# Kernel optimization log

Measured on AMD Instinct MI355X. Metric: run time of the kernel, lower is better.

Reference implementation:

```python
import jax, jax.numpy as jnp
import numpy as np

D_MODEL = 768
N_HEAD = 12
D_FF = 2048
KEEP_RATIO = 0.6
EPS = 1e-6


def rmsnorm(x, g):
    var = jnp.mean(x * x, axis=-1, keepdims=True)
    return x * jax.lax.rsqrt(var + EPS) * g


def setup_inputs() -> dict:
    key = jax.random.key(0)
    ks = jax.random.split(key, 16)
    B, S, D, F = 2, 2048, D_MODEL, D_FF
    s = 0.02
    inp = {
        "hidden": jax.random.normal(ks[0], (B, S, D), jnp.float32),
        "attn_mask": jnp.tril(jnp.ones((S, S), dtype=bool)),
        "temperature": 1,
        "wq": jax.random.normal(ks[1], (D, D), jnp.float32) * s,
        "wk": jax.random.normal(ks[2], (D, D), jnp.float32) * s,
        "wv": jax.random.normal(ks[3], (D, D), jnp.float32) * s,
        "wo": jax.random.normal(ks[4], (D, D), jnp.float32) * s,
        "w1": jax.random.normal(ks[5], (D, F), jnp.float32) * s,
        "w3": jax.random.normal(ks[6], (D, F), jnp.float32) * s,
        "w2": jax.random.normal(ks[7], (F, D), jnp.float32) * s,
        "g1": jnp.ones((D,), jnp.float32),
        "g2": jnp.ones((D,), jnp.float32),
        "w_mod": jax.random.normal(ks[8], (D,), jnp.float32) * s,
        "b_mod": jnp.zeros((), jnp.float32),
        "w_tok": jax.random.normal(ks[9], (D,), jnp.float32) * s,
        "b_tok": jnp.zeros((), jnp.float32),
        "w_gate": jax.random.normal(ks[10], (D, D), jnp.float32) * s,
        "b_gate": jnp.zeros((D,), jnp.float32),
    }
    return inp


def reference(hidden, attn_mask, temperature, wq, wk, wv, wo, w1, w3, w2,
              g1, g2, w_mod, b_mod, w_tok, b_tok, w_gate, b_gate):
    B, S, D = hidden.shape
    H = N_HEAD
    Dh = D // H

    # depth router: sigmoid(linear / temperature)
    depth_logits = jnp.einsum("bsd,d->bs", hidden, w_mod) + b_mod
    depth_probs = jax.nn.sigmoid(depth_logits / temperature)
    active = (depth_probs > 0.5).astype(hidden.dtype)[..., None]  # [B,S,1]

    normed = rmsnorm(hidden, g1)

    # token router: sigmoid scores, hard top-k keep mask at base keep ratio
    token_scores = jax.nn.sigmoid(jnp.einsum("bsd,d->bs", normed, w_tok) + b_tok)
    k = max(1, int(S * KEEP_RATIO))
    kth = jax.lax.top_k(token_scores, k)[0][:, -1:]  # [B,1]
    token_mask = (token_scores >= kth).astype(hidden.dtype)  # [B,S]

    # multi-head attention over normed
    q = jnp.einsum("bsd,de->bse", normed, wq).reshape(B, S, H, Dh)
    kk = jnp.einsum("bsd,de->bse", normed, wk).reshape(B, S, H, Dh)
    v = jnp.einsum("bsd,de->bse", normed, wv).reshape(B, S, H, Dh)
    logits = jnp.einsum("bqhd,bkhd->bhqk", q, kk) / jnp.sqrt(jnp.float32(Dh))
    logits = jnp.where(attn_mask[None, None, :, :], logits, jnp.float32(-1e9))
    probs = jax.nn.softmax(logits, axis=-1)
    ctx = jnp.einsum("bhqk,bkhd->bqhd", probs, v).reshape(B, S, D)
    attn_out = jnp.einsum("bsd,de->bse", ctx, wo)

    attn_out = attn_out * token_mask[..., None]
    hidden = hidden + attn_out * active  # dropout = identity (eval)

    # ACM gate: x * sigmoid(Wx + b)
    n2 = rmsnorm(hidden, g2)
    gated = n2 * jax.nn.sigmoid(jnp.einsum("bsd,de->bse", n2, w_gate) + b_gate)

    # SwiGLU MLP
    mlp = jnp.einsum("bsf,fd->bsd",
                     jax.nn.silu(jnp.einsum("bsd,df->bsf", gated, w1))
                     * jnp.einsum("bsd,df->bsf", gated, w3), w2)
    hidden = hidden + mlp * active
    return hidden, depth_probs, token_mask
```

## Files before the change

kernel.cpp:

```cpp
#include <hip/hip_runtime.h>


typedef float f32x4 __attribute__((ext_vector_type(4)));
typedef __bf16 bf16x8 __attribute__((ext_vector_type(8)));
typedef __bf16 bf16x4 __attribute__((ext_vector_type(4)));
typedef unsigned int u32;

#define DEV static __device__ __forceinline__

constexpr int SEQ = 2048, DIM = 768, NH = 12;
constexpr int KKEEP = 1228;

DEV f32x4 mfma16(bf16x8 a, bf16x8 b, f32x4 c) {
  return __builtin_amdgcn_mfma_f32_16x16x32_bf16(a, b, c, 0, 0, 0);
}
DEV float sigm(float x) { return 1.0f / (1.0f + __expf(-x)); }
DEV bf16x8 ld8(const __bf16* p) { return *reinterpret_cast<const bf16x8*>(p); }
DEV void st8(__bf16* p, bf16x8 v) { *reinterpret_cast<bf16x8*>(p) = v; }
DEV int swzo(int row, int u) { return row * 64 + ((u ^ (row & 7)) << 3); }

template <int NZ>
struct PtrPack { const float* s[NZ]; };

template <int NZ>
__global__ void k_transpose_castz(PtrPack<NZ> pp, __bf16* __restrict__ dst0,
                                  int K, int N, size_t dstride) {
  const float* __restrict__ src = pp.s[blockIdx.z];
  __bf16* __restrict__ dst = dst0 + (size_t)blockIdx.z * dstride;
  __shared__ float tile[32][33];
  const int tx = threadIdx.x, ty = threadIdx.y;
  const int n0 = blockIdx.x * 32, k0 = blockIdx.y * 32;
  for (int i = 0; i < 4; ++i)
    tile[ty + 8 * i][tx] = src[(size_t)(k0 + ty + 8 * i) * N + n0 + tx];
  __syncthreads();
  for (int i = 0; i < 4; ++i)
    dst[(size_t)(n0 + ty + 8 * i) * K + k0 + tx] = (__bf16)tile[tx][ty + 8 * i];
}

__global__ __launch_bounds__(256) void k_router(
    const float* __restrict__ hid, const float* __restrict__ g1,
    const float* __restrict__ wmod, const float* __restrict__ bmod,
    const float* __restrict__ wtok, const float* __restrict__ btok,
    const int* __restrict__ temp, __bf16* __restrict__ normed,
    float* __restrict__ depth_out, float* __restrict__ actF,
    float* __restrict__ tokL) {
  const int t = blockIdx.x, tid = threadIdx.x;
  const float* x = hid + (size_t)t * DIM;
  float xs[3], gs[3], ss = 0.f, dm = 0.f, dt = 0.f;
  for (int j = 0; j < 3; ++j) {
    const int i = tid + 256 * j;
    const float xv = x[i], g = g1[i];
    xs[j] = xv; gs[j] = g;
    ss += xv * xv;
    dm += xv * wmod[i];
    dt += xv * g * wtok[i];
  }
  for (int m = 32; m >= 1; m >>= 1) {
    ss += __shfl_xor(ss, m);
    dm += __shfl_xor(dm, m);
    dt += __shfl_xor(dt, m);
  }
  __shared__ float red[4][3];
  if ((tid & 63) == 0) { red[tid >> 6][0] = ss; red[tid >> 6][1] = dm; red[tid >> 6][2] = dt; }
  __syncthreads();
  ss = red[0][0] + red[1][0] + red[2][0] + red[3][0];
  dm = red[0][1] + red[1][1] + red[2][1] + red[3][1];
  dt = red[0][2] + red[1][2] + red[2][2] + red[3][2];
  const float rms = rsqrtf(ss / 768.0f + 1e-6f);
  if (tid == 0) {
    const int iv = temp[0];
    const float T = (iv > -100000 && iv < 100000) ? (float)iv : __int_as_float(iv);
    const float z = (dm + bmod[0]) / T;
    depth_out[t] = sigm(z);
    actF[t] = z > 0.0f ? 1.0f : 0.0f;
    tokL[t] = rms * dt + btok[0];
  }
  for (int j = 0; j < 3; ++j) {
    const int i = tid + 256 * j;
    normed[(size_t)t * DIM + i] = (__bf16)(xs[j] * rms * gs[j]);
  }
}

__global__ __launch_bounds__(256) void k_count(
    const float* __restrict__ tokL, float* __restrict__ kth_out) {
  const int b = blockIdx.y, tid = threadIdx.x;
  __shared__ float vals[2048];
  const float* L = tokL + (size_t)b * 2048;
#pragma unroll
  for (int j = 0; j < 8; ++j) vals[tid + 256 * j] = L[tid + 256 * j];
  __syncthreads();
  const int cand = blockIdx.x * 128 + (tid >> 1);
  const int half = tid & 1;
  const float e = vals[cand];
  int gt = 0, ge = 0;
  const float4* v4 = reinterpret_cast<const float4*>(vals) + half * 256;
#pragma unroll 8
  for (int j = 0; j < 256; ++j) {
    const float4 q = v4[j];
    gt += (q.x > e) + (q.y > e) + (q.z > e) + (q.w > e);
    ge += (q.x >= e) + (q.y >= e) + (q.z >= e) + (q.w >= e);
  }
  gt += __shfl_xor(gt, 1);
  ge += __shfl_xor(ge, 1);
  if (half == 0 && gt < KKEEP && KKEEP <= ge) kth_out[b] = e;
}

__global__ __launch_bounds__(256) void k_mask(
    const float* __restrict__ tokL, const float* __restrict__ kth,
    const float* __restrict__ actF, float* __restrict__ mask_out,
    float* __restrict__ maskact) {
  const int i = blockIdx.x * 256 + threadIdx.x;
  const int b = i >> 11;
  const float m = (tokL[i] >= kth[b]) ? 1.f : 0.f;
  mask_out[i] = m;
  maskact[i] = m * actF[i];
}

__global__ __launch_bounds__(256) void k_rmsnorm2(
    const float* __restrict__ h2, const float* __restrict__ g2,
    __bf16* __restrict__ n2) {
  const int t = blockIdx.x, tid = threadIdx.x;
  const float* x = h2 + (size_t)t * DIM;
  float xs[3], ss = 0.f;
  for (int j = 0; j < 3; ++j) { const float v = x[tid + 256 * j]; xs[j] = v; ss += v * v; }
  for (int m = 32; m >= 1; m >>= 1) ss += __shfl_xor(ss, m);
  __shared__ float red[4];
  if ((tid & 63) == 0) red[tid >> 6] = ss;
  __syncthreads();
  ss = red[0] + red[1] + red[2] + red[3];
  const float rms = rsqrtf(ss / 768.0f + 1e-6f);
  for (int j = 0; j < 3; ++j) {
    const int i = tid + 256 * j;
    n2[(size_t)t * DIM + i] = (__bf16)(xs[j] * rms * g2[i]);
  }
}

template <int EPI, int MI>
__global__ __launch_bounds__(256) void k_gemm(
    const __bf16* __restrict__ A, const __bf16* __restrict__ BT,
    int N, int K, size_t bt_stride, size_t out_stride,
    __bf16* __restrict__ outB, float* __restrict__ outF,
    const float* __restrict__ epF, const __bf16* __restrict__ epB,
    const float* __restrict__ rowsc, const float* __restrict__ bias) {
  constexpr int BM = MI * 32;
  __shared__ __align__(16) __bf16 As[BM * 64];
  __shared__ __align__(16) __bf16 Bs[128 * 64];
  const int tid = threadIdx.x;
  const int lane = tid & 63, w = tid >> 6;
  const int wr = w >> 1, wc = w & 1;
  const int f = lane & 15, e = lane >> 4;
  const int m0 = blockIdx.y * BM, n0 = blockIdx.x * 128;
  const __bf16* Bz = BT + (size_t)blockIdx.z * bt_stride;

  const int rowA = (MI == 4) ? (tid >> 1) : (tid >> 2);
  const int uA0  = (MI == 4) ? ((tid & 1) * 4) : ((tid & 3) * 2);
  const int rowB = tid >> 1, uB0 = (tid & 1) * 4;
  const __bf16* ApR = A + (size_t)(m0 + rowA) * K;
  const __bf16* BpR = Bz + (size_t)(n0 + rowB) * K;

  bf16x8 ya[MI], yb[4];
  auto LOADY = [&](int k0) {
#pragma unroll
    for (int j = 0; j < MI; ++j) ya[j] = ld8(ApR + k0 + (uA0 + j) * 8);
#pragma unroll
    for (int j = 0; j < 4; ++j) yb[j] = ld8(BpR + k0 + (uB0 + j) * 8);
  };
  auto STORE = [&]() {
#pragma unroll
    for (int j = 0; j < MI; ++j) st8(&As[swzo(rowA, uA0 + j)], ya[j]);
#pragma unroll
    for (int j = 0; j < 4; ++j) st8(&Bs[swzo(rowB, uB0 + j)], yb[j]);
  };

  f32x4 acc[MI][4] = {};
  LOADY(0);
  for (int k0 = 0; k0 < K; k0 += 64) {
    __syncthreads();
    STORE();
    if (k0 + 64 < K) LOADY(k0 + 64);
    __syncthreads();
    bf16x8 afl[MI], afh[MI], bfl[4], bfh[4];
#pragma unroll
    for (int mi = 0; mi < MI; ++mi) {
      const int row = wr * (MI * 16) + mi * 16 + f;
      afl[mi] = ld8(&As[swzo(row, e)]);
      afh[mi] = ld8(&As[swzo(row, e + 4)]);
    }
#pragma unroll
    for (int ni = 0; ni < 4; ++ni) {
      const int row = wc * 64 + ni * 16 + f;
      bfl[ni] = ld8(&Bs[swzo(row, e)]);
      bfh[ni] = ld8(&Bs[swzo(row, e + 4)]);
    }
#pragma unroll
    for (int mi = 0; mi < MI; ++mi)
#pragma unroll
      for (int ni = 0; ni < 4; ++ni) {
        acc[mi][ni] = mfma16(afl[mi], bfl[ni], acc[mi][ni]);
        acc[mi][ni] = mfma16(afh[mi], bfh[ni], acc[mi][ni]);
      }
  }
  const size_t oz = (size_t)blockIdx.z * out_stride;
  if constexpr (EPI == 5) {
    __bf16* vt = (__bf16*)outF;
    const bool isv = (blockIdx.z == 2);
#pragma unroll
    for (int mi = 0; mi < MI; ++mi)
#pragma unroll
      for (int ni = 0; ni < 4; ++ni) {
        const int row0 = m0 + wr * (MI * 16) + mi * 16 + e * 4;
        const int col = n0 + wc * 64 + ni * 16 + f;
        if (!isv) {
#pragma unroll
          for (int r2 = 0; r2 < 4; ++r2)
            outB[oz + (size_t)(row0 + r2) * N + col] = (__bf16)acc[mi][ni][r2];
        } else {
          bf16x4 pk;
#pragma unroll
          for (int r2 = 0; r2 < 4; ++r2) pk[r2] = (__bf16)acc[mi][ni][r2];
          *reinterpret_cast<bf16x4*>(&vt[(size_t)col * 4096 + row0]) = pk;
        }
      }
  } else {
#pragma unroll
    for (int mi = 0; mi < MI; ++mi)
#pragma unroll
      for (int ni = 0; ni < 4; ++ni)
#pragma unroll
        for (int r2 = 0; r2 < 4; ++r2) {
          const int row = m0 + wr * (MI * 16) + mi * 16 + e * 4 + r2;
          const int col = n0 + wc * 64 + ni * 16 + f;
          const size_t idx = (size_t)row * N + col;
          const float c = acc[mi][ni][r2];
          if constexpr (EPI == 0) {
            outB[oz + idx] = (__bf16)c;
          } else if constexpr (EPI == 1) {
            outF[idx] = epF[idx] + c * rowsc[row];
          } else if constexpr (EPI == 2) {
            outB[idx] = (__bf16)((float)epB[idx] * sigm(c + bias[col]));
          }
        }
  }
}

__global__ __launch_bounds__(256) void k_gemm13(
    const __bf16* __restrict__ A, const __bf16* __restrict__ B1T,
    const __bf16* __restrict__ B3T, __bf16* __restrict__ outT) {
  __shared__ __align__(16) __bf16 As[64 * 64];
  __shared__ __align__(16) __bf16 B1s[128 * 64];
  __shared__ __align__(16) __bf16 B3s[128 * 64];
  const int tid = threadIdx.x;
  const int lane = tid & 63, w = tid >> 6;
  const int wr = w >> 1, wc = w & 1;
  const int f = lane & 15, e = lane >> 4;
  const int m0 = blockIdx.y * 64, n0 = blockIdx.x * 128;
  const int rowA = tid >> 2, uA0 = (tid & 3) * 2;
  const int rowB = tid >> 1, uB0 = (tid & 1) * 4;
  const __bf16* ApR = A + (size_t)(m0 + rowA) * 768;
  const __bf16* B1R = B1T + (size_t)(n0 + rowB) * 768;
  const __bf16* B3R = B3T + (size_t)(n0 + rowB) * 768;

  bf16x8 ya[2], yb1[4], yb3[4];
  auto LOADY = [&](int k0) {
#pragma unroll
    for (int j = 0; j < 2; ++j) ya[j] = ld8(ApR + k0 + (uA0 + j) * 8);
#pragma unroll
    for (int j = 0; j < 4; ++j) yb1[j] = ld8(B1R + k0 + (uB0 + j) * 8);
#pragma unroll
    for (int j = 0; j < 4; ++j) yb3[j] = ld8(B3R + k0 + (uB0 + j) * 8);
  };
  auto STORE = [&]() {
#pragma unroll
    for (int j = 0; j < 2; ++j) st8(&As[swzo(rowA, uA0 + j)], ya[j]);
#pragma unroll
    for (int j = 0; j < 4; ++j) st8(&B1s[swzo(rowB, uB0 + j)], yb1[j]);
#pragma unroll
    for (int j = 0; j < 4; ++j) st8(&B3s[swzo(rowB, uB0 + j)], yb3[j]);
  };

  f32x4 acc1[2][4] = {}, acc3[2][4] = {};
  LOADY(0);
  for (int k0 = 0; k0 < 768; k0 += 64) {
    __syncthreads();
    STORE();
    if (k0 + 64 < 768) LOADY(k0 + 64);
    __syncthreads();
    bf16x8 afl[2], afh[2], bl[4], bh[4];
#pragma unroll
    for (int mi = 0; mi < 2; ++mi) {
      const int row = wr * 32 + mi * 16 + f;
      afl[mi] = ld8(&As[swzo(row, e)]);
      afh[mi] = ld8(&As[swzo(row, e + 4)]);
    }
#pragma unroll
    for (int ni = 0; ni < 4; ++ni) {
      const int row = wc * 64 + ni * 16 + f;
      bl[ni] = ld8(&B1s[swzo(row, e)]);
      bh[ni] = ld8(&B1s[swzo(row, e + 4)]);
    }
#pragma unroll
    for (int mi = 0; mi < 2; ++mi)
#pragma unroll
      for (int ni = 0; ni < 4; ++ni) {
        acc1[mi][ni] = mfma16(afl[mi], bl[ni], acc1[mi][ni]);
        acc1[mi][ni] = mfma16(afh[mi], bh[ni], acc1[mi][ni]);
      }
#pragma unroll
    for (int ni = 0; ni < 4; ++ni) {
      const int row = wc * 64 + ni * 16 + f;
      bl[ni] = ld8(&B3s[swzo(row, e)]);
      bh[ni] = ld8(&B3s[swzo(row, e + 4)]);
    }
#pragma unroll
    for (int mi = 0; mi < 2; ++mi)
#pragma unroll
      for (int ni = 0; ni < 4; ++ni) {
        acc3[mi][ni] = mfma16(afl[mi], bl[ni], acc3[mi][ni]);
        acc3[mi][ni] = mfma16(afh[mi], bh[ni], acc3[mi][ni]);
      }
  }
#pragma unroll
  for (int mi = 0; mi < 2; ++mi)
#pragma unroll
    for (int ni = 0; ni < 4; ++ni)
#pragma unroll
      for (int r2 = 0; r2 < 4; ++r2) {
        const int row = m0 + wr * 32 + mi * 16 + e * 4 + r2;
        const int col = n0 + wc * 64 + ni * 16 + f;
        const float u = acc1[mi][ni][r2];
        outT[(size_t)row * 2048 + col] = (__bf16)(u * sigm(u) * acc3[mi][ni][r2]);
      }
}

__global__ __launch_bounds__(256) void k_attn(
    const __bf16* __restrict__ qb, const __bf16* __restrict__ kb,
    const __bf16* __restrict__ vT, __bf16* __restrict__ Opart,
    float* __restrict__ ml) {
  __shared__ __bf16 Ks[64 * 64];
  __shared__ __bf16 Vt[64 * 64];
  __shared__ __bf16 Pl[4][16][72];
  const int tid = threadIdx.x, lane = tid & 63, w = tid >> 6;
  const int f = lane & 15, e = lane >> 4;
  const int idx = 79 - (int)blockIdx.x;
  int g4, rel;
  if (idx < 8)       { g4 = 0; rel = idx; }
  else if (idx < 24) { g4 = 1; rel = idx - 8; }
  else if (idx < 48) { g4 = 2; rel = idx - 24; }
  else               { g4 = 3; rel = idx - 48; }
  const int qt = (g4 << 3) + rel / (g4 + 1);
  const int c  = rel % (g4 + 1);
  const int bh = blockIdx.y;
  const int b = bh / NH, h = bh % NH;
  const int slot = bh * 80 + idx;
  const int q0 = qt * 64;
  const int kt0 = c * 8;
  const int ntile = min(8, qt + 1 - kt0);
  const size_t base = (size_t)b * SEQ * DIM + (size_t)h * 64;
  const float SCALE2 = 0.125f * 1.4426950408889634f;

  const int qrow = q0 + w * 16 + f;
  const bf16x8 aq0 = ld8(qb + base + (size_t)qrow * DIM + e * 8);
  const bf16x8 aq1 = ld8(qb + base + (size_t)qrow * DIM + 32 + e * 8);
  float lsum[4] = {0.f, 0.f, 0.f, 0.f};
  f32x4 cacc[4];
  for (int g = 0; g < 4; ++g) cacc[g] = f32x4{0.f, 0.f, 0.f, 0.f};

  const int r1 = tid >> 2, u0 = tid & 3;
  const __bf16* kp = kb + base + (size_t)r1 * DIM;
  const __bf16* vp = vT + (size_t)(h * 64 + r1) * 4096 + b * 2048;

  bf16x8 rk0 = ld8(kp + (size_t)(kt0 * 64) * DIM + u0 * 8);
  bf16x8 rk1 = ld8(kp + (size_t)(kt0 * 64) * DIM + (u0 + 4) * 8);
  bf16x8 rv0 = ld8(vp + kt0 * 64 + u0 * 8);
  bf16x8 rv1 = ld8(vp + kt0 * 64 + (u0 + 4) * 8);

  for (int tt = 0; tt < ntile; ++tt) {
    const int kt = kt0 + tt;
    __syncthreads();
    st8(&Ks[swzo(r1, u0)], rk0);  st8(&Ks[swzo(r1, u0 + 4)], rk1);
    st8(&Vt[swzo(r1, u0)], rv0);  st8(&Vt[swzo(r1, u0 + 4)], rv1);
    if (tt + 1 < ntile) {
      const size_t ko = (size_t)((kt + 1) * 64) * DIM;
      rk0 = ld8(kp + ko + u0 * 8);  rk1 = ld8(kp + ko + (u0 + 4) * 8);
      const int vo = (kt + 1) * 64;
      rv0 = ld8(vp + vo + u0 * 8);  rv1 = ld8(vp + vo + (u0 + 4) * 8);
    }
    __syncthreads();

    f32x4 sacc[4];
#pragma unroll
    for (int g = 0; g < 4; ++g) {
      const int row = g * 16 + f;
      f32x4 z = f32x4{0.f, 0.f, 0.f, 0.f};
      z = mfma16(aq0, ld8(&Ks[swzo(row, e)]), z);
      z = mfma16(aq1, ld8(&Ks[swzo(row, e + 4)]), z);
      sacc[g] = z;
    }
    const bool need_mask = (kt == qt);
    const int qg = q0 + w * 16 + e * 4;
    float p[4][4];
#pragma unroll
    for (int g = 0; g < 4; ++g) {
      const int kg = kt * 64 + g * 16 + f;
#pragma unroll
      for (int r = 0; r < 4; ++r) {
        const float pv = (need_mask && (kg > qg + r))
                             ? 0.f
                             : exp2f(sacc[g][r] * SCALE2);
        p[g][r] = pv;
        lsum[r] += pv;
      }
    }
#pragma unroll
    for (int g = 0; g < 4; ++g)
#pragma unroll
      for (int r = 0; r < 4; ++r) Pl[w][e * 4 + r][g * 16 + f] = (__bf16)p[g][r];
    const bf16x8 ap0 = ld8(&Pl[w][f][e * 8]);
    const bf16x8 ap1 = ld8(&Pl[w][f][32 + e * 8]);
#pragma unroll
    for (int g = 0; g < 4; ++g) {
      const int row = g * 16 + f;
      cacc[g] = mfma16(ap0, ld8(&Vt[swzo(row, e)]), cacc[g]);
      cacc[g] = mfma16(ap1, ld8(&Vt[swzo(row, e + 4)]), cacc[g]);
    }
  }
  for (int m = 1; m < 16; m <<= 1)
#pragma unroll
    for (int r = 0; r < 4; ++r) lsum[r] += __shfl_xor(lsum[r], m);
  if (f == 0) {
#pragma unroll
    for (int r = 0; r < 4; ++r)
      ml[(size_t)slot * 64 + w * 16 + e * 4 + r] = lsum[r];
  }
#pragma unroll
  for (int g = 0; g < 4; ++g)
#pragma unroll
    for (int r = 0; r < 4; ++r) {
      const int row = w * 16 + e * 4 + r;
      Opart[(size_t)slot * 4096 + row * 64 + g * 16 + f] = (__bf16)cacc[g][r];
    }
}

__global__ __launch_bounds__(256) void k_attn_combine(
    const __bf16* __restrict__ Opart, const float* __restrict__ ml,
    __bf16* __restrict__ ctxb) {
  const int qt = blockIdx.x, bh = blockIdx.y;
  const int b = bh / NH, h = bh % NH;
  const int g = qt >> 3;
  const int sb = bh * 80 + 4 * g * (g + 1) + (qt & 7) * (g + 1);
  const int nch = g + 1;
  const int row = threadIdx.x >> 2, dh0 = (threadIdx.x & 3) * 16;

  float ltot = 0.f;
  float acc[16];
#pragma unroll
  for (int j = 0; j < 16; ++j) acc[j] = 0.f;
  for (int cc = 0; cc < nch; ++cc) {
    ltot += ml[(size_t)(sb + cc) * 64 + row];
    const __bf16* op = Opart + (size_t)(sb + cc) * 4096 + row * 64 + dh0;
    const bf16x8 o0 = ld8(op), o1 = ld8(op + 8);
#pragma unroll
    for (int j = 0; j < 8; ++j) {
      acc[j] += (float)o0[j];
      acc[8 + j] += (float)o1[j];
    }
  }
  const float rl = 1.0f / ltot;
  bf16x8 w0, w1;
#pragma unroll
  for (int j = 0; j < 8; ++j) {
    w0[j] = (__bf16)(acc[j] * rl);
    w1[j] = (__bf16)(acc[8 + j] * rl);
  }
  const size_t base = (size_t)b * SEQ * DIM + (size_t)h * 64;
  __bf16* dst = ctxb + base + (size_t)(qt * 64 + row) * DIM + dh0;
  st8(dst, w0);
  st8(dst + 8, w1);
}

extern "C" void kernel_launch(void* const* d_in, const int* in_sizes, int n_in,
                              void* d_out, int out_size, void* d_ws, size_t ws_size,
                              hipStream_t stream) {
  const float* hid   = (const float*)d_in[0];
  const int*   temp  = (const int*)d_in[2];
  const float* wq    = (const float*)d_in[3];
  const float* wk    = (const float*)d_in[4];
  const float* wv    = (const float*)d_in[5];
  const float* wo    = (const float*)d_in[6];
  const float* w1    = (const float*)d_in[7];
  const float* w3    = (const float*)d_in[8];
  const float* w2    = (const float*)d_in[9];
  const float* g1    = (const float*)d_in[10];
  const float* g2    = (const float*)d_in[11];
  const float* wmod  = (const float*)d_in[12];
  const float* bmod  = (const float*)d_in[13];
  const float* wtok  = (const float*)d_in[14];
  const float* btok  = (const float*)d_in[15];
  const float* wgate = (const float*)d_in[16];
  const float* bgate = (const float*)d_in[17];

  char* ws = (char*)d_ws;
  __bf16* WT = (__bf16*)ws;
  const size_t oWQ = 0, oWK = 589824, oWV = 1179648, oWO = 1769472,
               oWG = 2359296, oW1 = 2949120, oW3 = 4521984, oW2 = 6094848;
  __bf16* qbuf   = (__bf16*)(ws + 15335424);
  __bf16* kbuf   = qbuf + 3145728;
  __bf16* vTbuf  = kbuf + 3145728;
  __bf16* normed = (__bf16*)(ws + 34209792);
  __bf16* ctxb   = normed + 3145728;
  __bf16* n2buf  = ctxb + 3145728;
  __bf16* tbuf   = normed;
  float*  h2     = (float*)(ws + 53084160);
  __bf16* gated  = (__bf16*)(ws + 65667072);
  __bf16* Opart  = (__bf16*)(ws + 53084160);
  float*  mlbuf  = (float*)(ws + 68812800);
  float*  tokL   = (float*)(ws + 71958528);
  float*  actF   = tokL + 4096;
  float*  maskact = actF + 4096;
  float*  kthbuf  = maskact + 4096;

  float* dout = (float*)d_out;
  float* out_hidden = dout;
  float* out_depth  = dout + 3145728;
  float* out_mask   = dout + 3145728 + 4096;

  const dim3 tb(32, 8);
  PtrPack<5> p5; p5.s[0]=wq; p5.s[1]=wk; p5.s[2]=wv; p5.s[3]=wo; p5.s[4]=wgate;
  k_transpose_castz<5><<<dim3(24, 24, 5), tb, 0, stream>>>(p5, WT + oWQ, 768, 768, 589824);
  PtrPack<2> p2; p2.s[0]=w1; p2.s[1]=w3;
  k_transpose_castz<2><<<dim3(64, 24, 2), tb, 0, stream>>>(p2, WT + oW1, 768, 2048, 1572864);
  PtrPack<1> p1; p1.s[0]=w2;
  k_transpose_castz<1><<<dim3(24, 64, 1), tb, 0, stream>>>(p1, WT + oW2, 2048, 768, 0);

  k_router<<<4096, 256, 0, stream>>>(hid, g1, wmod, bmod, wtok, btok, temp,
                                     normed, out_depth, actF, tokL);
  k_count<<<dim3(16, 2), 256, 0, stream>>>(tokL, kthbuf);
  k_mask<<<16, 256, 0, stream>>>(tokL, kthbuf, actF, out_mask, maskact);

  k_gemm<5, 4><<<dim3(6, 32, 3), 256, 0, stream>>>(
      normed, WT + oWQ, 768, 768, 589824, 3145728,
      qbuf, (float*)vTbuf, nullptr, nullptr, nullptr, nullptr);

  k_attn<<<dim3(80, 24), 256, 0, stream>>>(qbuf, kbuf, vTbuf, Opart, mlbuf);
  k_attn_combine<<<dim3(32, 24), 256, 0, stream>>>(Opart, mlbuf, ctxb);

  k_gemm<1, 2><<<dim3(6, 64, 1), 256, 0, stream>>>(
      ctxb, WT + oWO, 768, 768, 0, 0,
      nullptr, h2, hid, nullptr, maskact, nullptr);

  k_rmsnorm2<<<4096, 256, 0, stream>>>(h2, g2, n2buf);

  k_gemm<2, 2><<<dim3(6, 64, 1), 256, 0, stream>>>(
      n2buf, WT + oWG, 768, 768, 0, 0,
      gated, nullptr, nullptr, n2buf, nullptr, bgate);

  k_gemm13<<<dim3(16, 64), 256, 0, stream>>>(gated, WT + oW1, WT + oW3, tbuf);

  k_gemm<1, 2><<<dim3(6, 64, 1), 256, 0, stream>>>(
      tbuf, WT + oW2, 768, 2048, 0, 0,
      nullptr, out_hidden, h2, nullptr, actF, nullptr);

  (void)in_sizes; (void)n_in; (void)out_size; (void)ws_size;
}
```

Baseline: 205.2 us.

## Enlarge fused W1/W3 GEMM tile to 128x128 and fold softmax scale into Q

```diff
diff --git a/kernel.cpp b/kernel.cpp
--- a/kernel.cpp
+++ b/kernel.cpp
@@ -10,6 +10,7 @@
 
 constexpr int SEQ = 2048, DIM = 768, NH = 12;
 constexpr int KKEEP = 1228;
+constexpr float SCALE2 = 0.125f * 1.4426950408889634f;
 
 DEV f32x4 mfma16(bf16x8 a, bf16x8 b, f32x4 c) {
   return __builtin_amdgcn_mfma_f32_16x16x32_bf16(a, b, c, 0, 0, 0);
@@ -18,6 +19,7 @@
 DEV bf16x8 ld8(const __bf16* p) { return *reinterpret_cast<const bf16x8*>(p); }
 DEV void st8(__bf16* p, bf16x8 v) { *reinterpret_cast<bf16x8*>(p) = v; }
 DEV int swzo(int row, int u) { return row * 64 + ((u ^ (row & 7)) << 3); }
+DEV int swz32(int row, int u) { return row * 32 + ((u ^ (row & 3)) << 3); }
 
 template <int NZ>
 struct PtrPack { const float* s[NZ]; };
@@ -204,6 +206,7 @@
   if constexpr (EPI == 5) {
     __bf16* vt = (__bf16*)outF;
     const bool isv = (blockIdx.z == 2);
+    const float qs = (blockIdx.z == 0) ? SCALE2 : 1.0f;
 #pragma unroll
     for (int mi = 0; mi < MI; ++mi)
 #pragma unroll
@@ -213,7 +216,8 @@
         if (!isv) {
 #pragma unroll
           for (int r2 = 0; r2 < 4; ++r2)
-            outB[oz + (size_t)(row0 + r2) * N + col] = (__bf16)acc[mi][ni][r2];
+            outB[oz + (size_t)(row0 + r2) * N + col] =
+                (__bf16)(acc[mi][ni][r2] * qs);
         } else {
           bf16x4 pk;
 #pragma unroll
@@ -246,86 +250,72 @@
 __global__ __launch_bounds__(256) void k_gemm13(
     const __bf16* __restrict__ A, const __bf16* __restrict__ B1T,
     const __bf16* __restrict__ B3T, __bf16* __restrict__ outT) {
-  __shared__ __align__(16) __bf16 As[64 * 64];
-  __shared__ __align__(16) __bf16 B1s[128 * 64];
-  __shared__ __align__(16) __bf16 B3s[128 * 64];
+  __shared__ __align__(16) __bf16 As[128 * 32];
+  __shared__ __align__(16) __bf16 B1s[128 * 32];
+  __shared__ __align__(16) __bf16 B3s[128 * 32];
   const int tid = threadIdx.x;
   const int lane = tid & 63, w = tid >> 6;
   const int wr = w >> 1, wc = w & 1;
   const int f = lane & 15, e = lane >> 4;
-  const int m0 = blockIdx.y * 64, n0 = blockIdx.x * 128;
-  const int rowA = tid >> 2, uA0 = (tid & 3) * 2;
-  const int rowB = tid >> 1, uB0 = (tid & 1) * 4;
-  const __bf16* ApR = A + (size_t)(m0 + rowA) * 768;
-  const __bf16* B1R = B1T + (size_t)(n0 + rowB) * 768;
-  const __bf16* B3R = B3T + (size_t)(n0 + rowB) * 768;
-
-  bf16x8 ya[2], yb1[4], yb3[4];
+  const int m0 = blockIdx.y * 128, n0 = blockIdx.x * 128;
+  const int rowS = tid >> 1, uS = (tid & 1) * 2;
+  const __bf16* ApR = A + (size_t)(m0 + rowS) * 768;
+  const __bf16* B1R = B1T + (size_t)(n0 + rowS) * 768;
+  const __bf16* B3R = B3T + (size_t)(n0 + rowS) * 768;
+
+  bf16x8 ya[2], yb1[2], yb3[2];
   auto LOADY = [&](int k0) {
 #pragma unroll
-    for (int j = 0; j < 2; ++j) ya[j] = ld8(ApR + k0 + (uA0 + j) * 8);
-#pragma unroll
-    for (int j = 0; j < 4; ++j) yb1[j] = ld8(B1R + k0 + (uB0 + j) * 8);
-#pragma unroll
-    for (int j = 0; j < 4; ++j) yb3[j] = ld8(B3R + k0 + (uB0 + j) * 8);
+    for (int j = 0; j < 2; ++j) {
+      ya[j] = ld8(ApR + k0 + (uS + j) * 8);
+      yb1[j] = ld8(B1R + k0 + (uS + j) * 8);
+      yb3[j] = ld8(B3R + k0 + (uS + j) * 8);
+    }
   };
   auto STORE = [&]() {
 #pragma unroll
-    for (int j = 0; j < 2; ++j) st8(&As[swzo(rowA, uA0 + j)], ya[j]);
-#pragma unroll
-    for (int j = 0; j < 4; ++j) st8(&B1s[swzo(rowB, uB0 + j)], yb1[j]);
-#pragma unroll
-    for (int j = 0; j < 4; ++j) st8(&B3s[swzo(rowB, uB0 + j)], yb3[j]);
+    for (int j = 0; j < 2; ++j) {
+      st8(&As[swz32(rowS, uS + j)], ya[j]);
+      st8(&B1s[swz32(rowS, uS + j)], yb1[j]);
+      st8(&B3s[swz32(rowS, uS + j)], yb3[j]);
+    }
   };
 
-  f32x4 acc1[2][4] = {}, acc3[2][4] = {};
+  f32x4 acc1[4][4] = {}, acc3[4][4] = {};
   LOADY(0);
-  for (int k0 = 0; k0 < 768; k0 += 64) {
+  for (int k0 = 0; k0 < 768; k0 += 32) {
     __syncthreads();
     STORE();
-    if (k0 + 64 < 768) LOADY(k0 + 64);
+    if (k0 + 32 < 768) LOADY(k0 + 32);
     __syncthreads();
-    bf16x8 afl[2], afh[2], bl[4], bh[4];
-#pragma unroll
-    for (int mi = 0; mi < 2; ++mi) {
-      const int row = wr * 32 + mi * 16 + f;
-      afl[mi] = ld8(&As[swzo(row, e)]);
-      afh[mi] = ld8(&As[swzo(row, e + 4)]);
-    }
-#pragma unroll
-    for (int ni = 0; ni < 4; ++ni) {
-      const int row = wc * 64 + ni * 16 + f;
-      bl[ni] = ld8(&B1s[swzo(row, e)]);
-      bh[ni] = ld8(&B1s[swzo(row, e + 4)]);
-    }
-#pragma unroll
-    for (int mi = 0; mi < 2; ++mi)
-#pragma unroll
-      for (int ni = 0; ni < 4; ++ni) {
-        acc1[mi][ni] = mfma16(afl[mi], bl[ni], acc1[mi][ni]);
-        acc1[mi][ni] = mfma16(afh[mi], bh[ni], acc1[mi][ni]);
-      }
-#pragma unroll
-    for (int ni = 0; ni < 4; ++ni) {
-      const int row = wc * 64 + ni * 16 + f;
-      bl[ni] = ld8(&B3s[swzo(row, e)]);
-      bh[ni] = ld8(&B3s[swzo(row, e + 4)]);
-    }
-#pragma unroll
-    for (int mi = 0; mi < 2; ++mi)
-#pragma unroll
-      for (int ni = 0; ni < 4; ++ni) {
-        acc3[mi][ni] = mfma16(afl[mi], bl[ni], acc3[mi][ni]);
-        acc3[mi][ni] = mfma16(afh[mi], bh[ni], acc3[mi][ni]);
-      }
-  }
-#pragma unroll
-  for (int mi = 0; mi < 2; ++mi)
+    bf16x8 af[4], bb[4];
+#pragma unroll
+    for (int mi = 0; mi < 4; ++mi)
+      af[mi] = ld8(&As[swz32(wr * 64 + mi * 16 + f, e)]);
 #pragma unroll
     for (int ni = 0; ni < 4; ++ni)
+      bb[ni] = ld8(&B1s[swz32(wc * 64 + ni * 16 + f, e)]);
+#pragma unroll
+    for (int mi = 0; mi < 4; ++mi)
+#pragma unroll
+      for (int ni = 0; ni < 4; ++ni)
+        acc1[mi][ni] = mfma16(af[mi], bb[ni], acc1[mi][ni]);
+#pragma unroll
+    for (int ni = 0; ni < 4; ++ni)
+      bb[ni] = ld8(&B3s[swz32(wc * 64 + ni * 16 + f, e)]);
+#pragma unroll
+    for (int mi = 0; mi < 4; ++mi)
+#pragma unroll
+      for (int ni = 0; ni < 4; ++ni)
+        acc3[mi][ni] = mfma16(af[mi], bb[ni], acc3[mi][ni]);
+  }
+#pragma unroll
+  for (int mi = 0; mi < 4; ++mi)
+#pragma unroll
+    for (int ni = 0; ni < 4; ++ni)
 #pragma unroll
       for (int r2 = 0; r2 < 4; ++r2) {
-        const int row = m0 + wr * 32 + mi * 16 + e * 4 + r2;
+        const int row = m0 + wr * 64 + mi * 16 + e * 4 + r2;
         const int col = n0 + wc * 64 + ni * 16 + f;
         const float u = acc1[mi][ni][r2];
         outT[(size_t)row * 2048 + col] = (__bf16)(u * sigm(u) * acc3[mi][ni][r2]);
@@ -356,7 +346,6 @@
   const int kt0 = c * 8;
   const int ntile = min(8, qt + 1 - kt0);
   const size_t base = (size_t)b * SEQ * DIM + (size_t)h * 64;
-  const float SCALE2 = 0.125f * 1.4426950408889634f;
 
   const int qrow = q0 + w * 16 + f;
   const bf16x8 aq0 = ld8(qb + base + (size_t)qrow * DIM + e * 8);
@@ -406,7 +395,7 @@
       for (int r = 0; r < 4; ++r) {
         const float pv = (need_mask && (kg > qg + r))
                              ? 0.f
-                             : exp2f(sacc[g][r] * SCALE2);
+                             : exp2f(sacc[g][r]);
         p[g][r] = pv;
         lsum[r] += pv;
       }
@@ -554,7 +543,7 @@
       n2buf, WT + oWG, 768, 768, 0, 0,
       gated, nullptr, nullptr, n2buf, nullptr, bgate);
 
-  k_gemm13<<<dim3(16, 64), 256, 0, stream>>>(gated, WT + oW1, WT + oW3, tbuf);
+  k_gemm13<<<dim3(16, 32), 256, 0, stream>>>(gated, WT + oW1, WT + oW3, tbuf);
 
   k_gemm<1, 2><<<dim3(6, 64, 1), 256, 0, stream>>>(
       tbuf, WT + oW2, 768, 2048, 0, 0,
```

Measured after the change: 208.1 us. Within noise of the previous version (+1.4%).
